# Kernel tuning notes

Hardware: AMD Instinct MI355X
Metric: run time of the kernel (lower is better)

The kernel has to match this reference:

```python
import jax, jax.numpy as jnp
import numpy as np

N = 50000      # nodes
E = 800000     # edges (avg degree 16)
B = 8          # graphs in batch
H = 128        # hidden (message_passer out_channels)
FF = 64        # fourier_feat_dim -> fourier features have dim 2*FF
REPEATS = 4    # repeats_training
OUT = 4        # output_dim
IN_X = 5
IN_MASK = 3

def _fourier(x, M):
    # https://arxiv.org/pdf/2106.02795.pdf : [cos(xM), sin(xM)] / sqrt(2F)
    p = x @ M
    return jnp.concatenate([jnp.cos(p), jnp.sin(p)], axis=-1) / jnp.sqrt(2.0 * M.shape[1])

def _seg_mean(v, idx, n):
    s = jax.ops.segment_sum(v, idx, num_segments=n)
    c = jax.ops.segment_sum(jnp.ones((v.shape[0],), v.dtype), idx, num_segments=n)
    return s / jnp.maximum(c, 1.0)[:, None]

def setup_inputs() -> dict:
    key = jax.random.key(0)
    ks = jax.random.split(key, 16)
    x = jax.random.normal(ks[0], (N, IN_X), jnp.float32)
    x_mask = jax.random.bernoulli(ks[1], 0.1, (N, IN_MASK)).astype(jnp.float32)
    edge_index = jax.random.randint(ks[2], (2, E), 0, N)
    edge_attr = jax.random.normal(ks[3], (E, 3), jnp.float32)
    pos = jax.random.uniform(ks[4], (N, 2), jnp.float32)
    batch = jnp.sort(jax.random.randint(ks[5], (N,), 0, B))
    sampling_points = jax.random.uniform(ks[6], (2,), jnp.float32)
    fourier_mat = jax.random.normal(ks[7], (2, FF), jnp.float32)  # learnable, init N(0,1)
    W_enc = jax.random.normal(ks[8], (IN_X + IN_MASK, H), jnp.float32) * 0.1
    b_enc = jnp.zeros((H,), jnp.float32)
    W_msg = jax.random.normal(ks[9], (2 * H + 3, H), jnp.float32) * 0.05
    b_msg = jnp.zeros((H,), jnp.float32)
    W_upd = jax.random.normal(ks[10], (4 * H, H), jnp.float32) * 0.05
    b_upd = jnp.zeros((H,), jnp.float32)
    W_dec = jax.random.normal(ks[11], (H, OUT), jnp.float32) * 0.1
    b_dec = jnp.zeros((OUT,), jnp.float32)
    return dict(x=x, x_mask=x_mask, edge_index=edge_index, edge_attr=edge_attr,
                pos=pos, batch=batch, sampling_points=sampling_points,
                fourier_mat=fourier_mat, W_enc=W_enc, b_enc=b_enc,
                W_msg=W_msg, b_msg=b_msg, W_upd=W_upd, b_upd=b_upd,
                W_dec=W_dec, b_dec=b_dec)

def reference(x, x_mask, edge_index, edge_attr, pos, batch, sampling_points,
              fourier_mat, W_enc, b_enc, W_msg, b_msg, W_upd, b_upd, W_dec, b_dec):
    bc = x_mask[:, -1]                                   # 0/1 BC flag
    x_full = jnp.concatenate([x, x_mask], axis=1)        # x = concat([x, x_mask])
    keys_ff = _fourier(pos, fourier_mat)                 # input fourier features [N, 2F]
    h = jax.nn.relu(x_full @ W_enc + b_enc)              # encoder -> [N, H]

    # x_BC: scatter-mean over BC nodes per graph (computed once)
    bc_sum = jax.ops.segment_sum(h * bc[:, None], batch, num_segments=B)
    bc_cnt = jax.ops.segment_sum(bc, batch, num_segments=B)
    x_BC = bc_sum / jnp.maximum(bc_cnt, 1.0)[:, None]    # [B, H]

    x_graph = _seg_mean(h, batch, B)                     # global_mean_pool [B, H]
    src, dst = edge_index[0], edge_index[1]
    deg = jnp.maximum(jax.ops.segment_sum(jnp.ones((E,), h.dtype), dst, num_segments=N), 1.0)

    for _ in range(REPEATS):  # repeated message passing
        m = jax.nn.relu(jnp.concatenate([h[src], h[dst], edge_attr], axis=1) @ W_msg + b_msg)
        agg = jax.ops.segment_sum(m, dst, num_segments=N) / deg[:, None]  # scatter-mean
        upd_in = jnp.concatenate([h, agg, x_graph[batch], x_BC[batch]], axis=1)
        h = h + jax.nn.relu(upd_in @ W_upd + b_upd)
        x_graph = _seg_mean(h, batch, B)                 # re-pool each repeat

    decoded = h @ W_dec + b_dec                          # [N, OUT]

    # kernelized fourier-feature interpolation at the sampling point
    q = _fourier(sampling_points, fourier_mat)           # [2F]
    nq = q / jnp.linalg.norm(q)
    nk = keys_ff / jnp.linalg.norm(keys_ff, axis=1, keepdims=True)
    vals_sum = h.sum(axis=0)                             # [H]
    kwv = nk.T @ h                                       # [2F, H]
    ks_sum = nk.sum(axis=0)                              # [2F]
    enc = (vals_sum + nq @ kwv) / (N + nq @ ks_sum)      # [H]
    U_sampled = enc @ W_dec + b_dec                      # [OUT]
    # pack (U_sampled, decoded) into one array: row 0 = sampled point, rows 1: = nodes
    return jnp.concatenate([U_sampled[None, :], decoded], axis=0)
```

## Files before the change

kernel.cpp:

```cpp
#include <hip/hip_runtime.h>
#include <math.h>

#define Nn 50000
#define Ee 800000
#define Bb 8
#define ROUNDS 4
#define KWVB 512
#define SCB 196
#define AP 40
#define HP 132
#define KS 40
#define HTT 136
#define NBK 196
#define P1B 391
#define CHUNK 2047

typedef __attribute__((ext_vector_type(8))) short bf16x8;
typedef __attribute__((ext_vector_type(4))) float f32x4;

__device__ inline short f2bf(float f) {
  union { float f; unsigned u; } v; v.f = f;
  unsigned r = v.u + 0x7fff + ((v.u >> 16) & 1);
  return (short)(r >> 16);
}
__device__ inline float bf2f(short s) {
  union { float f; unsigned u; } v; v.u = ((unsigned)(unsigned short)s) << 16;
  return v.f;
}

__global__ __launch_bounds__(256) void encode_seg(
    const float* __restrict__ x, const float* __restrict__ xm,
    const int* __restrict__ batch, const float* __restrict__ W,
    const float* __restrict__ b, float* __restrict__ h,
    float* __restrict__ gsum, float* __restrict__ gcnt,
    float* __restrict__ bcsum, float* __restrict__ bccnt) {
  __shared__ float xs5[128 * 5];
  __shared__ float xm3[128 * 3];
  __shared__ float ls[Bb * 128];
  __shared__ float lb[Bb * 128];
  __shared__ float lc[Bb], lbc[Bb];
  const int t = threadIdx.x;
  const int nBase = blockIdx.x * 128;
  const int j = t & 127, half = t >> 7;
  const int base5 = nBase * 5, base3 = nBase * 3;
  for (int q = t; q < 640; q += 256) xs5[q] = (base5 + q < Nn * 5) ? x[base5 + q] : 0.f;
  for (int q = t; q < 384; q += 256) xm3[q] = (base3 + q < Nn * 3) ? xm[base3 + q] : 0.f;
  for (int q = t; q < Bb * 128; q += 256) { ls[q] = 0.f; lb[q] = 0.f; }
  if (t < Bb) { lc[t] = 0.f; lbc[t] = 0.f; }
  float Wcol[8];
#pragma unroll
  for (int k = 0; k < 8; k++) Wcol[k] = W[k * 128 + j];
  const float bj = b[j];
  __syncthreads();
  int curb = -1;
  float runh = 0.f, runb = 0.f, runc = 0.f, runbc = 0.f;
  for (int kk = 0; kk < 64; kk++) {
    int i = nBase + kk * 2 + half;
    if (i >= Nn) break;
    int li = i - nBase;
    float acc = bj;
#pragma unroll
    for (int k = 0; k < 5; k++) acc = fmaf(xs5[li * 5 + k], Wcol[k], acc);
#pragma unroll
    for (int k = 0; k < 3; k++) acc = fmaf(xm3[li * 3 + k], Wcol[5 + k], acc);
    float v = fmaxf(acc, 0.f);
    h[(size_t)i * 128 + j] = v;
    float bc = xm3[li * 3 + 2];
    int g = batch[i];
    if (g != curb) {
      if (curb >= 0) {
        atomicAdd(&ls[curb * 128 + j], runh);
        atomicAdd(&lb[curb * 128 + j], runb);
        if (j == 0) { atomicAdd(&lc[curb], runc); atomicAdd(&lbc[curb], runbc); }
      }
      curb = g; runh = runb = runc = runbc = 0.f;
    }
    runh += v; runb += v * bc;
    if (j == 0) { runc += 1.f; runbc += bc; }
  }
  if (curb >= 0) {
    atomicAdd(&ls[curb * 128 + j], runh);
    atomicAdd(&lb[curb * 128 + j], runb);
    if (j == 0) { atomicAdd(&lc[curb], runc); atomicAdd(&lbc[curb], runbc); }
  }
  __syncthreads();
  for (int q = t; q < Bb * 128; q += 256) {
    float a = ls[q], c = lb[q];
    if (a != 0.f) atomicAdd(&gsum[q], a);
    if (c != 0.f) atomicAdd(&bcsum[q], c);
  }
  if (t < Bb) { atomicAdd(&gcnt[t], lc[t]); atomicAdd(&bccnt[t], lbc[t]); }
}

__global__ __launch_bounds__(256) void bkt_cnt(
    const int* __restrict__ ei, int* __restrict__ bktcnt,
    const float* __restrict__ Wm, const float* __restrict__ Wu,
    short* __restrict__ Wmt_h, short* __restrict__ Wmt_l,
    short* __restrict__ Wut_h, short* __restrict__ Wut_l) {
  __shared__ int hist[NBK];
  int t = threadIdx.x;
  int idx = blockIdx.x * 256 + t;
  if (idx < 32768) {
    int k = idx & 127, n = (idx >> 7) & 127, y = idx >> 14;
    float w = Wm[(size_t)(y * 128 + k) * 128 + n];
    short hi = f2bf(w);
    Wmt_h[idx] = hi;
    Wmt_l[idx] = f2bf(w - bf2f(hi));
  } else if (idx < 65536) {
    int j = idx - 32768;
    int k = j & 255, n = j >> 8;
    float w = Wu[(size_t)k * 128 + n];
    short hi = f2bf(w);
    Wut_h[j] = hi;
    Wut_l[j] = f2bf(w - bf2f(hi));
  }
  for (int q = t; q < NBK; q += 256) hist[q] = 0;
  __syncthreads();
  int base = blockIdx.x * CHUNK;
  int end = base + CHUNK < Ee ? base + CHUNK : Ee;
  for (int e = base + t; e < end; e += 256) atomicAdd(&hist[ei[Ee + e] >> 8], 1);
  __syncthreads();
  for (int q = t; q < NBK; q += 256)
    if (hist[q]) atomicAdd(&bktcnt[q], hist[q]);
}
__global__ __launch_bounds__(256) void bkt_scan(const int* __restrict__ bktcnt,
                                                int* __restrict__ bktbase,
                                                int* __restrict__ bktcur) {
  __shared__ int s[256];
  int t = threadIdx.x;
  int v = (t < NBK) ? bktcnt[t] : 0;
  s[t] = v;
  __syncthreads();
  for (int off = 1; off < 256; off <<= 1) {
    int x = (t >= off) ? s[t - off] : 0;
    __syncthreads();
    s[t] += x;
    __syncthreads();
  }
  int ex = s[t] - v;
  if (t < NBK) { bktbase[t] = ex; bktcur[t] = ex; }
  if (t == NBK - 1) bktbase[NBK] = ex + v;
}
__global__ __launch_bounds__(256) void bkt_part(
    const int* __restrict__ ei, const float* __restrict__ ea,
    int* __restrict__ bktcur, int2* __restrict__ recA,
    unsigned char* __restrict__ dlo) {
  __shared__ int hist[NBK], lbase[NBK], lcur[NBK];
  int t = threadIdx.x;
  for (int q = t; q < NBK; q += 256) hist[q] = 0;
  __syncthreads();
  int base = blockIdx.x * CHUNK;
  int end = base + CHUNK < Ee ? base + CHUNK : Ee;
  for (int e = base + t; e < end; e += 256) atomicAdd(&hist[ei[Ee + e] >> 8], 1);
  __syncthreads();
  for (int q = t; q < NBK; q += 256) {
    int c = hist[q];
    lbase[q] = c ? atomicAdd(&bktcur[q], c) : 0;
    lcur[q] = 0;
  }
  __syncthreads();
  for (int e = base + t; e < end; e += 256) {
    int d = ei[Ee + e];
    int bk = d >> 8;
    int p = lbase[bk] + atomicAdd(&lcur[bk], 1);
    unsigned r0 = (unsigned)ei[e] |
                  ((unsigned)(unsigned short)f2bf(ea[3 * (size_t)e + 0]) << 16);
    unsigned r1 = (unsigned)(unsigned short)f2bf(ea[3 * (size_t)e + 1]) |
                  ((unsigned)(unsigned short)f2bf(ea[3 * (size_t)e + 2]) << 16);
    recA[p] = make_int2((int)r0, (int)r1);
    dlo[p] = (unsigned char)(d & 255);
  }
}
__global__ __launch_bounds__(256) void dst_cnt_bsum(
    const int* __restrict__ bktbase, const unsigned char* __restrict__ dlo,
    int* __restrict__ cnt, int* __restrict__ bsum) {
  __shared__ int hh[256];
  __shared__ int wsum[4];
  int t = threadIdx.x;
  hh[t] = 0;
  __syncthreads();
  int b = blockIdx.x;
  int lo = bktbase[b], hi = bktbase[b + 1];
  for (int i = lo + t; i < hi; i += 256) atomicAdd(&hh[dlo[i]], 1);
  __syncthreads();
  int d = b * 256 + t;
  int v = hh[t];
  if (d < Nn) cnt[d] = v;
#pragma unroll
  for (int off = 32; off > 0; off >>= 1) v += __shfl_down(v, off);
  if ((t & 63) == 0) wsum[t >> 6] = v;
  __syncthreads();
  if (t == 0) bsum[b] = wsum[0] + wsum[1] + wsum[2] + wsum[3];
}
__global__ __launch_bounds__(256) void scan_top_kernel(const int* __restrict__ bsum,
                                                       int* __restrict__ boff) {
  __shared__ int s[256];
  int t = threadIdx.x;
  int v = (t < SCB) ? bsum[t] : 0;
  s[t] = v;
  __syncthreads();
  for (int off = 1; off < 256; off <<= 1) {
    int x = (t >= off) ? s[t - off] : 0;
    __syncthreads();
    s[t] += x;
    __syncthreads();
  }
  boff[t] = s[t] - v;
}
__global__ __launch_bounds__(256) void apply_fin(
    const int* __restrict__ cnt, const int* __restrict__ boff,
    const int* __restrict__ bktbase, const int2* __restrict__ recA,
    const unsigned char* __restrict__ dlo,
    int* __restrict__ rowptr, float* __restrict__ invdeg,
    int2* __restrict__ rec) {
  __shared__ int s[256];
  __shared__ int cur[256];
  int t = threadIdx.x, b = blockIdx.x;
  int i = b * 256 + t;
  int v = (i < Nn) ? cnt[i] : 0;
  s[t] = v;
  __syncthreads();
  for (int off = 1; off < 256; off <<= 1) {
    int x = (t >= off) ? s[t - off] : 0;
    __syncthreads();
    s[t] += x;
    __syncthreads();
  }
  int ex = boff[b] + s[t] - v;
  if (i < Nn) {
    rowptr[i] = ex;
    invdeg[i] = 1.0f / fmaxf((float)v, 1.0f);
    if (i == Nn - 1) rowptr[Nn] = ex + v;
  }
  cur[t] = ex;
  __syncthreads();
  int lo = bktbase[b], hi = bktbase[b + 1];
  for (int ii = lo + t; ii < hi; ii += 256) {
    int dl = dlo[ii];
    int p = atomicAdd(&cur[dl], 1);
    rec[p] = recA[ii];
  }
}

__global__ __launch_bounds__(256) void proj_mfma(
    const float* __restrict__ h, const short* __restrict__ Wth,
    unsigned char* __restrict__ hs8, unsigned short* __restrict__ hdbf,
    const float* __restrict__ bcsum, const float* __restrict__ bccnt,
    const float* __restrict__ bu, const float* __restrict__ Wu,
    float* __restrict__ gbst, const float* __restrict__ gsum_in,
    const float* __restrict__ gcnt, float* __restrict__ gb_out) {
  __shared__ short Ah_s[64 * AP];
  __shared__ short Bh_s[256 * AP];
  const int t = threadIdx.x;
  const int nBase = blockIdx.x * 64;
  const int wave = t >> 6, lane = t & 63;
  const int ml = lane & 15, quad = lane >> 4;
  const int ko = quad * 8;

  if (blockIdx.x < Bb) {
    float* xgs = (float*)Bh_s;
    const int g = blockIdx.x;
    if (t < 128) xgs[t] = bcsum[g * 128 + t] / fmaxf(bccnt[g], 1.f);
    __syncthreads();
    if (t < 128) {
      float a = bu[t];
#pragma unroll 4
      for (int k = 0; k < 128; k++) a = fmaf(xgs[k], Wu[(size_t)(384 + k) * 128 + t], a);
      gbst[g * 128 + t] = a;
    }
    __syncthreads();
    if (t < 128) xgs[t] = gsum_in[g * 128 + t] / fmaxf(gcnt[g], 1.f);
    __syncthreads();
    if (t < 128) {
      float a = gbst[g * 128 + t];
#pragma unroll 4
      for (int k = 0; k < 128; k++) a = fmaf(xgs[k], Wu[(size_t)(256 + k) * 128 + t], a);
      gb_out[g * 128 + t] = a;
    }
  }

  f32x4 acc[4][4];
#pragma unroll
  for (int yn = 0; yn < 4; yn++)
#pragma unroll
    for (int mt = 0; mt < 4; mt++)
#pragma unroll
      for (int q = 0; q < 4; q++) acc[yn][mt][q] = 0.f;

  const int arow = t >> 2;
  const int kq = (t & 3) * 8;
  const int nd0 = nBase + arow;
  const int nn = nd0 < Nn ? nd0 : Nn - 1;

  for (int c = 0; c < 4; c++) {
    const int k0 = c * 32;
    const float* p = &h[(size_t)nn * 128 + k0 + kq];
    float4 u0 = *(const float4*)(p + 0);
    float4 u1 = *(const float4*)(p + 4);
    const bf16x8 w0 = *(const bf16x8*)&Wth[(size_t)t * 128 + k0];
    const bf16x8 w1 = *(const bf16x8*)&Wth[(size_t)t * 128 + k0 + 8];
    const bf16x8 w2 = *(const bf16x8*)&Wth[(size_t)t * 128 + k0 + 16];
    const bf16x8 w3 = *(const bf16x8*)&Wth[(size_t)t * 128 + k0 + 24];
    float xs[8] = {u0.x, u0.y, u0.z, u0.w, u1.x, u1.y, u1.z, u1.w};
    bf16x8 vh0;
#pragma unroll
    for (int j = 0; j < 8; j++) vh0[j] = f2bf(xs[j]);
    __syncthreads();
    *(bf16x8*)&Ah_s[arow * AP + kq] = vh0;
    *(bf16x8*)&Bh_s[t * AP + 0] = w0;
    *(bf16x8*)&Bh_s[t * AP + 8] = w1;
    *(bf16x8*)&Bh_s[t * AP + 16] = w2;
    *(bf16x8*)&Bh_s[t * AP + 24] = w3;
    __syncthreads();
#pragma unroll
    for (int mt = 0; mt < 4; mt++) {
      const int ar = (mt * 16 + ml) * AP + ko;
      bf16x8 ah = *(const bf16x8*)&Ah_s[ar];
#pragma unroll
      for (int y = 0; y < 2; y++) {
#pragma unroll
        for (int nt = 0; nt < 2; nt++) {
          const int br = (y * 128 + wave * 32 + nt * 16 + ml) * AP + ko;
          bf16x8 bh = *(const bf16x8*)&Bh_s[br];
          acc[y * 2 + nt][mt] = __builtin_amdgcn_mfma_f32_16x16x32_bf16(ah, bh, acc[y * 2 + nt][mt], 0, 0, 0);
        }
      }
    }
  }
#pragma unroll
  for (int nt = 0; nt < 2; nt++) {
    const int ch = wave * 32 + nt * 16 + ml;
#pragma unroll
    for (int mt = 0; mt < 4; mt++) {
#pragma unroll
      for (int q = 0; q < 4; q++) {
        int nd = nBase + mt * 16 + quad * 4 + q;
        if (nd < Nn) {
          int pk = __builtin_amdgcn_cvt_pk_fp8_f32(acc[nt][mt][q], acc[nt][mt][q], 0, false);
          hs8[(size_t)nd * 128 + ch] = (unsigned char)(pk & 0xff);
          hdbf[(size_t)nd * 128 + ch] = (unsigned short)f2bf(acc[2 + nt][mt][q]);
        }
      }
    }
  }
}

__global__ __launch_bounds__(256) void agg_kernel(
    const unsigned char* __restrict__ hs8, const unsigned short* __restrict__ hdbf,
    unsigned short* __restrict__ aggbf, const int2* __restrict__ rec,
    const int* __restrict__ rowptr, const float* __restrict__ invdeg,
    const float* __restrict__ Wm, const float* __restrict__ bm,
    const float* __restrict__ Wu, const float* __restrict__ gbst,
    const float* __restrict__ gsum_in, const float* __restrict__ gcnt,
    float* __restrict__ gb_out, int dogb) {
  __shared__ float xgs[128];
  int t = threadIdx.x;
  if (dogb && blockIdx.x < Bb) {
    const int g = blockIdx.x;
    if (t < 128) xgs[t] = gsum_in[g * 128 + t] / fmaxf(gcnt[g], 1.f);
    __syncthreads();
    if (t < 128) {
      float a = gbst[g * 128 + t];
#pragma unroll 4
      for (int k = 0; k < 128; k++) a = fmaf(xgs[k], Wu[(size_t)(256 + k) * 128 + t], a);
      gb_out[g * 128 + t] = a;
    }
  }
  int hw = t >> 5, lane = t & 31;
  int v = blockIdx.x * 8 + hw;
  if (v >= Nn) return;
  int c0 = lane * 4;
  const float4 We0 = *(const float4*)&Wm[(size_t)256 * 128 + c0];
  const float4 We1 = *(const float4*)&Wm[(size_t)257 * 128 + c0];
  const float4 We2 = *(const float4*)&Wm[(size_t)258 * 128 + c0];
  const float4 b4  = *(const float4*)&bm[c0];
  const ushort4 hd4 = *(const ushort4*)&hdbf[(size_t)v * 128 + c0];
// ... 33 lines not shown
  }
  if (e < r1) {
    int2 q0 = rec[e];
    int s0 = q0.x & 0xffff;
    unsigned hr0 = *(const unsigned*)&hs8[(size_t)s0 * 128 + c0];
    float e00 = bf2f((short)(q0.x >> 16));
    float e01 = bf2f((short)(q0.y & 0xffff));
    float e02 = bf2f((short)(q0.y >> 16));
    float h0x = __builtin_amdgcn_cvt_f32_fp8(hr0, 0);
    float h0y = __builtin_amdgcn_cvt_f32_fp8(hr0, 1);
    float h0z = __builtin_amdgcn_cvt_f32_fp8(hr0, 2);
    float h0w = __builtin_amdgcn_cvt_f32_fp8(hr0, 3);
    ax += fmaxf(fmaf(e00, We0.x, fmaf(e01, We1.x, fmaf(e02, We2.x, h0x + bx))), 0.f);
    ay += fmaxf(fmaf(e00, We0.y, fmaf(e01, We1.y, fmaf(e02, We2.y, h0y + by))), 0.f);
    az += fmaxf(fmaf(e00, We0.z, fmaf(e01, We1.z, fmaf(e02, We2.z, h0z + bz))), 0.f);
    aw += fmaxf(fmaf(e00, We0.w, fmaf(e01, We1.w, fmaf(e02, We2.w, h0w + bw))), 0.f);
  }
  const float idg = invdeg[v];
  ushort4 o;
  o.x = (unsigned short)f2bf((ax + ax2) * idg);
  o.y = (unsigned short)f2bf((ay + ay2) * idg);
  o.z = (unsigned short)f2bf((az + az2) * idg);
  o.w = (unsigned short)f2bf((aw + aw2) * idg);
  *(ushort4*)&aggbf[(size_t)v * 128 + c0] = o;
}

__global__ __launch_bounds__(256) void updg_proj(
    float* __restrict__ h, const unsigned short* __restrict__ aggbf,
    const int* __restrict__ batch,
    const short* __restrict__ Wth, const short* __restrict__ Wtl,
    const float* __restrict__ gb, float* __restrict__ gsum_out,
    const short* __restrict__ Wmth, unsigned char* __restrict__ hs8,
    unsigned short* __restrict__ hdbf, int doproj) {
  __shared__ short ms[15360];
  __shared__ float gbs[Bb * 128];
  __shared__ float ls[Bb * 128];
  short* Ah_s = ms;
  short* Al_s = ms + 64 * AP;
  short* Bh_s = ms + 2 * 64 * AP;
  short* Bl_s = ms + 2 * 64 * AP + 128 * AP;
  short* hnT  = ms;

  const int t = threadIdx.x;
  const int nBase = blockIdx.x * 64;
  *(float4*)&gbs[t * 4] = *(const float4*)&gb[t * 4];
#pragma unroll
  for (int q = 0; q < 4; q++) ls[t + q * 256] = 0.f;

  const int wave = t >> 6, lane = t & 63;
  const int ml = lane & 15, quad = lane >> 4;
  const int ko = quad * 8;

  f32x4 acc[2][4];
#pragma unroll
  for (int nt = 0; nt < 2; nt++)
#pragma unroll
    for (int mt = 0; mt < 4; mt++)
#pragma unroll
      for (int q = 0; q < 4; q++) acc[nt][mt][q] = 0.f;

  const int arow = t >> 2;
  const int kq = (t & 3) * 8;
  const int brow = t >> 1;
  const int kc = (t & 1) * 16;
  const int nd0 = nBase + arow;
  const int nn = nd0 < Nn ? nd0 : Nn - 1;

  for (int c = 0; c < 8; c++) {
    const int k0 = c * 32;
    bf16x8 vh0, vl0;
    if (c < 4) {
      const float* p = &h[(size_t)nn * 128 + k0 + kq];
      float4 u0 = *(const float4*)(p + 0);
      float4 u1 = *(const float4*)(p + 4);
      float xs[8] = {u0.x, u0.y, u0.z, u0.w, u1.x, u1.y, u1.z, u1.w};
#pragma unroll
      for (int j = 0; j < 8; j++) {
        short hi = f2bf(xs[j]);
        vh0[j] = hi; vl0[j] = f2bf(xs[j] - bf2f(hi));
      }
    } else {
      vh0 = *(const bf16x8*)&aggbf[(size_t)nn * 128 + (c - 4) * 32 + kq];
    }
    const bf16x8 gb0 = *(const bf16x8*)&Wth[(size_t)brow * 256 + k0 + kc];
    const bf16x8 gb1 = *(const bf16x8*)&Wth[(size_t)brow * 256 + k0 + kc + 8];
    const bf16x8 gl0 = *(const bf16x8*)&Wtl[(size_t)brow * 256 + k0 + kc];
    const bf16x8 gl1 = *(const bf16x8*)&Wtl[(size_t)brow * 256 + k0 + kc + 8];
    __syncthreads();
    *(bf16x8*)&Ah_s[arow * AP + kq] = vh0;
    if (c < 4) *(bf16x8*)&Al_s[arow * AP + kq] = vl0;
    *(bf16x8*)&Bh_s[brow * AP + kc] = gb0;
    *(bf16x8*)&Bh_s[brow * AP + kc + 8] = gb1;
    *(bf16x8*)&Bl_s[brow * AP + kc] = gl0;
    *(bf16x8*)&Bl_s[brow * AP + kc + 8] = gl1;
    __syncthreads();
    if (c < 4) {
#pragma unroll
      for (int mt = 0; mt < 4; mt++) {
        const int ar = (mt * 16 + ml) * AP + ko;
        bf16x8 ah = *(const bf16x8*)&Ah_s[ar];
        bf16x8 al = *(const bf16x8*)&Al_s[ar];
#pragma unroll
        for (int nt = 0; nt < 2; nt++) {
          const int br = (wave * 32 + nt * 16 + ml) * AP + ko;
          bf16x8 bh = *(const bf16x8*)&Bh_s[br];
          bf16x8 bl = *(const bf16x8*)&Bl_s[br];
          acc[nt][mt] = __builtin_amdgcn_mfma_f32_16x16x32_bf16(ah, bh, acc[nt][mt], 0, 0, 0);
          acc[nt][mt] = __builtin_amdgcn_mfma_f32_16x16x32_bf16(ah, bl, acc[nt][mt], 0, 0, 0);
          acc[nt][mt] = __builtin_amdgcn_mfma_f32_16x16x32_bf16(al, bh, acc[nt][mt], 0, 0, 0);
        }
      }
    } else {
#pragma unroll
      for (int mt = 0; mt < 4; mt++) {
        const int ar = (mt * 16 + ml) * AP + ko;
        bf16x8 ah = *(const bf16x8*)&Ah_s[ar];
#pragma unroll
        for (int nt = 0; nt < 2; nt++) {
          const int br = (wave * 32 + nt * 16 + ml) * AP + ko;
          bf16x8 bh = *(const bf16x8*)&Bh_s[br];
          bf16x8 bl = *(const bf16x8*)&Bl_s[br];
          acc[nt][mt] = __builtin_amdgcn_mfma_f32_16x16x32_bf16(ah, bh, acc[nt][mt], 0, 0, 0);
          acc[nt][mt] = __builtin_amdgcn_mfma_f32_16x16x32_bf16(ah, bl, acc[nt][mt], 0, 0, 0);
        }
      }
    }
  }
  __syncthreads();

#pragma unroll
  for (int nt = 0; nt < 2; nt++) {
    const int ch = wave * 32 + nt * 16 + ml;
#pragma unroll
    for (int mt = 0; mt < 4; mt++) {
      int lrb = mt * 16 + quad * 4;
      int rbase = nBase + lrb;
      float runv = 0.f;
      int curb = -1;
#pragma unroll
      for (int q = 0; q < 4; q++) {
        int nd = rbase + q;
        short hv = 0;
        if (nd < Nn) {
          int bi = batch[nd];
          float u = fmaxf(acc[nt][mt][q] + gbs[bi * 128 + ch], 0.f);
          float hn = h[(size_t)nd * 128 + ch] + u;
          h[(size_t)nd * 128 + ch] = hn;
          hv = f2bf(hn);
          if (bi != curb) {
            if (curb >= 0) atomicAdd(&ls[curb * 128 + ch], runv);
            curb = bi;
            runv = 0.f;
          }
          runv += hn;
        }
        hnT[(lrb + q) * HTT + ch] = hv;
      }
      if (curb >= 0) atomicAdd(&ls[curb * 128 + ch], runv);
// ... 238 lines not shown
                              void* d_out, int out_size, void* d_ws, size_t ws_size,
                              hipStream_t stream) {
  const float* x    = (const float*)d_in[0];
  const float* xm   = (const float*)d_in[1];
  const int*   ei   = (const int*)d_in[2];
  const float* ea   = (const float*)d_in[3];
  const float* pos  = (const float*)d_in[4];
  const int*   batch= (const int*)d_in[5];
  const float* sp   = (const float*)d_in[6];
  const float* Fm   = (const float*)d_in[7];
  const float* Wenc = (const float*)d_in[8];
  const float* benc = (const float*)d_in[9];
  const float* Wmsg = (const float*)d_in[10];
  const float* bmsg = (const float*)d_in[11];
  const float* Wupd = (const float*)d_in[12];
  const float* bupd = (const float*)d_in[13];
  const float* Wdec = (const float*)d_in[14];
  const float* bdec = (const float*)d_in[15];
  float* out = (float*)d_out;

  float* ws     = (float*)d_ws;
  float* h      = ws;
  float* agg    = h + (size_t)Nn * 128;
  float* aux    = agg + (size_t)Nn * 128;
  float* invdeg = aux + (size_t)Nn * 128;
  float* gsum   = invdeg + Nn;
  float* gcnt   = gsum + 1024;
  float* bcsum  = gcnt + 8;
  float* bccnt  = bcsum + 1024;
  float* gsumR  = bccnt + 8;
  float* vsum   = gsumR + 4096;
  float* ksum   = vsum + 128;
  int*   bktcnt = (int*)(ksum + 128);
  float* gbst   = (float*)(bktcnt + 196);
  float* gbuf   = gbst + 1024;
  float* kwv    = gbuf + 4096;
  int2*  rec    = (int2*)(kwv + 16384);
  int*   cnt    = (int*)(rec + Ee);
  int*   rowptr = cnt + Nn;
  int*   bsum   = rowptr + Nn + 1;
  int*   boff   = bsum + 256;
  int*   bktbase= boff + 256;
  int*   bktcur = bktbase + 197;
  short* wmt_h  = (short*)(bktcur + 196);
  short* wmt_l  = wmt_h + 32768;
  short* wut_h  = wmt_l + 32768;
  short* wut_l  = wut_h + 32768;
  int2*  recA   = (int2*)(wut_l + 32768);
  unsigned char* dlo = (unsigned char*)(recA + Ee);

  unsigned short* aggbf = (unsigned short*)agg;
  unsigned char*  hs8   = (unsigned char*)aux;
  unsigned short* hdbf  = (unsigned short*)(hs8 + (size_t)Nn * 128);

  hipMemsetAsync(gsum, 0, 6612 * 4, stream);

  bkt_cnt<<<P1B, 256, 0, stream>>>(ei, bktcnt, Wmsg, Wupd,
                                   wmt_h, wmt_l, wut_h, wut_l);
  bkt_scan<<<1, 256, 0, stream>>>(bktcnt, bktbase, bktcur);
  bkt_part<<<P1B, 256, 0, stream>>>(ei, ea, bktcur, recA, dlo);
  dst_cnt_bsum<<<NBK, 256, 0, stream>>>(bktbase, dlo, cnt, bsum);
  scan_top_kernel<<<1, 256, 0, stream>>>(bsum, boff);
  apply_fin<<<NBK, 256, 0, stream>>>(cnt, boff, bktbase, recA, dlo,
                                     rowptr, invdeg, rec);

  const int nb128 = (Nn + 127) / 128;
  const int nb64  = (Nn + 63) / 64;
  encode_seg<<<nb128, 256, 0, stream>>>(x, xm, batch, Wenc, benc, h,
                                        gsum, gcnt, bcsum, bccnt);

  proj_mfma<<<nb64, 256, 0, stream>>>(h, wmt_h, hs8, hdbf,
                                      bcsum, bccnt, bupd, Wupd, gbst,
                                      gsum, gcnt, gbuf);

  for (int r = 0; r < ROUNDS; r++) {
    agg_kernel<<<(Nn + 7) / 8, 256, 0, stream>>>(
        hs8, hdbf, aggbf, rec, rowptr, invdeg, Wmsg, bmsg,
        Wupd, gbst,
        (r == 0) ? gsum : (gsumR + (size_t)(r - 1) * 1024), gcnt,
        gbuf + (size_t)r * 1024, (r >= 1) ? 1 : 0);
    updg_proj<<<nb64, 256, 0, stream>>>(
        h, aggbf, batch, wut_h, wut_l,
        gbuf + (size_t)r * 1024, gsumR + (size_t)r * 1024,
        wmt_h, hs8, hdbf, (r < ROUNDS - 1) ? 1 : 0);
  }

  kwv_kernel<<<KWVB, 256, 0, stream>>>(h, pos, Fm, Wdec, bdec, agg, ksum, out);
  kwv_reduce<<<64, 256, 0, stream>>>(agg, kwv);
  final_kernel<<<1, 128, 0, stream>>>(sp, Fm, kwv, gsumR + 3 * 1024, ksum,
                                      Wdec, bdec, out);
}
```

Measured before the change: 617.8 us.

## Stage full A tile in LDS once and load weight fragments directly from global

In proj_mfma and updg_proj, the per-32-k-chunk loop that staged both the activation and weight tiles into LDS with two barriers per chunk is replaced. The whole 64x128 activation tile (hi/lo bf16 split) is now written to padded LDS once, and the MFMA B fragments are read straight from global (L2-cached) weights. proj_mfma also splits its two 128-wide outputs into a sequential loop to cut accumulator registers. This removes most __syncthreads and LDS weight traffic, in exchange for uncoalesced per-lane global weight loads and more LDS per block.

Result: no change. 626.4 us (+1.4%).

```diff
diff --git a/kernel.cpp b/kernel.cpp
--- a/kernel.cpp
+++ b/kernel.cpp
@@ -7,7 +7,6 @@
 #define ROUNDS 4
 #define KWVB 512
 #define SCB 196
-#define AP 40
 #define HP 132
 #define KS 40
 #define HTT 136
@@ -249,8 +248,7 @@
     const float* __restrict__ bu, const float* __restrict__ Wu,
     float* __restrict__ gbst, const float* __restrict__ gsum_in,
     const float* __restrict__ gcnt, float* __restrict__ gb_out) {
-  __shared__ short Ah_s[64 * AP];
-  __shared__ short Bh_s[256 * AP];
+  __shared__ short Ah[64 * HTT];
   const int t = threadIdx.x;
   const int nBase = blockIdx.x * 64;
   const int wave = t >> 6, lane = t & 63;
@@ -258,7 +256,7 @@
   const int ko = quad * 8;
 
   if (blockIdx.x < Bb) {
-    float* xgs = (float*)Bh_s;
+    float* xgs = (float*)Ah;
     const int g = blockIdx.x;
     if (t < 128) xgs[t] = bcsum[g * 128 + t] / fmaxf(bccnt[g], 1.f);
     __syncthreads();
@@ -277,68 +275,76 @@
       for (int k = 0; k < 128; k++) a = fmaf(xgs[k], Wu[(size_t)(256 + k) * 128 + t], a);
       gb_out[g * 128 + t] = a;
     }
-  }
-
-  f32x4 acc[4][4];
-#pragma unroll
-  for (int yn = 0; yn < 4; yn++)
-#pragma unroll
-    for (int mt = 0; mt < 4; mt++)
-#pragma unroll
-      for (int q = 0; q < 4; q++) acc[yn][mt][q] = 0.f;
-
-  const int arow = t >> 2;
-  const int kq = (t & 3) * 8;
-  const int nd0 = nBase + arow;
+    __syncthreads();
+  }
+
+  const int ar = t >> 2;
+  const int cb = (t & 3) * 32;
+  const int nd0 = nBase + ar;
   const int nn = nd0 < Nn ? nd0 : Nn - 1;
 
-  for (int c = 0; c < 4; c++) {
-    const int k0 = c * 32;
-    const float* p = &h[(size_t)nn * 128 + k0 + kq];
-    float4 u0 = *(const float4*)(p + 0);
-    float4 u1 = *(const float4*)(p + 4);
-    const bf16x8 w0 = *(const bf16x8*)&Wth[(size_t)t * 128 + k0];
-    const bf16x8 w1 = *(const bf16x8*)&Wth[(size_t)t * 128 + k0 + 8];
-    const bf16x8 w2 = *(const bf16x8*)&Wth[(size_t)t * 128 + k0 + 16];
-    const bf16x8 w3 = *(const bf16x8*)&Wth[(size_t)t * 128 + k0 + 24];
-    float xs[8] = {u0.x, u0.y, u0.z, u0.w, u1.x, u1.y, u1.z, u1.w};
-    bf16x8 vh0;
-#pragma unroll
-    for (int j = 0; j < 8; j++) vh0[j] = f2bf(xs[j]);
-    __syncthreads();
-    *(bf16x8*)&Ah_s[arow * AP + kq] = vh0;
-    *(bf16x8*)&Bh_s[t * AP + 0] = w0;
-    *(bf16x8*)&Bh_s[t * AP + 8] = w1;
-    *(bf16x8*)&Bh_s[t * AP + 16] = w2;
-    *(bf16x8*)&Bh_s[t * AP + 24] = w3;
-    __syncthreads();
-#pragma unroll
-    for (int mt = 0; mt < 4; mt++) {
-      const int ar = (mt * 16 + ml) * AP + ko;
-      bf16x8 ah = *(const bf16x8*)&Ah_s[ar];
-#pragma unroll
-      for (int y = 0; y < 2; y++) {
-#pragma unroll
-        for (int nt = 0; nt < 2; nt++) {
-          const int br = (y * 128 + wave * 32 + nt * 16 + ml) * AP + ko;
-          bf16x8 bh = *(const bf16x8*)&Bh_s[br];
-          acc[y * 2 + nt][mt] = __builtin_amdgcn_mfma_f32_16x16x32_bf16(ah, bh, acc[y * 2 + nt][mt], 0, 0, 0);
+  {
+    const float* p = &h[(size_t)nn * 128 + cb];
+#pragma unroll
+    for (int jj = 0; jj < 4; jj++) {
+      float4 u0 = *(const float4*)(p + jj * 8);
+      float4 u1 = *(const float4*)(p + jj * 8 + 4);
+      float xs[8] = {u0.x, u0.y, u0.z, u0.w, u1.x, u1.y, u1.z, u1.w};
+      bf16x8 vh;
+#pragma unroll
+      for (int j = 0; j < 8; j++) vh[j] = f2bf(xs[j]);
+      *(bf16x8*)&Ah[ar * HTT + cb + jj * 8] = vh;
+    }
+  }
+  __syncthreads();
+
+#pragma unroll 1
+  for (int y = 0; y < 2; y++) {
+    f32x4 pacc[2][4];
+#pragma unroll
+    for (int nt = 0; nt < 2; nt++)
+#pragma unroll
+      for (int mt = 0; mt < 4; mt++)
+#pragma unroll
+        for (int q = 0; q < 4; q++) pacc[nt][mt][q] = 0.f;
+#pragma unroll
+    for (int c = 0; c < 4; c++) {
+      const bf16x8 b0 = *(const bf16x8*)&Wth[(size_t)(y * 128 + wave * 32 + ml) * 128 + c * 32 + ko];
+      const bf16x8 b1 = *(const bf16x8*)&Wth[(size_t)(y * 128 + wave * 32 + 16 + ml) * 128 + c * 32 + ko];
+#pragma unroll
+      for (int mt = 0; mt < 4; mt++) {
+        bf16x8 ah = *(const bf16x8*)&Ah[(mt * 16 + ml) * HTT + c * 32 + ko];
+        pacc[0][mt] = __builtin_amdgcn_mfma_f32_16x16x32_bf16(ah, b0, pacc[0][mt], 0, 0, 0);
+        pacc[1][mt] = __builtin_amdgcn_mfma_f32_16x16x32_bf16(ah, b1, pacc[1][mt], 0, 0, 0);
+      }
+    }
+    if (y == 0) {
+#pragma unroll
+      for (int nt = 0; nt < 2; nt++) {
+        const int ch = wave * 32 + nt * 16 + ml;
+#pragma unroll
+        for (int mt = 0; mt < 4; mt++) {
+#pragma unroll
+          for (int q = 0; q < 4; q++) {
+            int nd = nBase + mt * 16 + quad * 4 + q;
+            if (nd < Nn) {
+              int pk = __builtin_amdgcn_cvt_pk_fp8_f32(pacc[nt][mt][q], pacc[nt][mt][q], 0, false);
+              hs8[(size_t)nd * 128 + ch] = (unsigned char)(pk & 0xff);
+            }
+          }
         }
       }
-    }
-  }
-#pragma unroll
-  for (int nt = 0; nt < 2; nt++) {
-    const int ch = wave * 32 + nt * 16 + ml;
-#pragma unroll
-    for (int mt = 0; mt < 4; mt++) {
-#pragma unroll
-      for (int q = 0; q < 4; q++) {
-        int nd = nBase + mt * 16 + quad * 4 + q;
-        if (nd < Nn) {
-          int pk = __builtin_amdgcn_cvt_pk_fp8_f32(acc[nt][mt][q], acc[nt][mt][q], 0, false);
-          hs8[(size_t)nd * 128 + ch] = (unsigned char)(pk & 0xff);
-          hdbf[(size_t)nd * 128 + ch] = (unsigned short)f2bf(acc[2 + nt][mt][q]);
+    } else {
+#pragma unroll
+      for (int nt = 0; nt < 2; nt++) {
+        const int ch = wave * 32 + nt * 16 + ml;
+#pragma unroll
+        for (int mt = 0; mt < 4; mt++) {
+#pragma unroll
+          for (int q = 0; q < 4; q++) {
+            int nd = nBase + mt * 16 + quad * 4 + q;
+            if (nd < Nn) hdbf[(size_t)nd * 128 + ch] = (unsigned short)f2bf(pacc[nt][mt][q]);
+          }
         }
       }
     }
@@ -441,14 +447,12 @@
     const float* __restrict__ gb, float* __restrict__ gsum_out,
     const short* __restrict__ Wmth, unsigned char* __restrict__ hs8,
     unsigned short* __restrict__ hdbf, int doproj) {
-  __shared__ short ms[15360];
+  __shared__ short ms[2 * 64 * HTT];
   __shared__ float gbs[Bb * 128];
   __shared__ float ls[Bb * 128];
-  short* Ah_s = ms;
-  short* Al_s = ms + 64 * AP;
-  short* Bh_s = ms + 2 * 64 * AP;
-  short* Bl_s = ms + 2 * 64 * AP + 128 * AP;
-  short* hnT  = ms;
+  short* Ah = ms;
+  short* Al = ms + 64 * HTT;
+  short* hnT = ms;
 
   const int t = threadIdx.x;
   const int nBase = blockIdx.x * 64;
@@ -468,71 +472,73 @@
 #pragma unroll
       for (int q = 0; q < 4; q++) acc[nt][mt][q] = 0.f;
 
-  const int arow = t >> 2;
-  const int kq = (t & 3) * 8;
-  const int brow = t >> 1;
-  const int kc = (t & 1) * 16;
-  const int nd0 = nBase + arow;
+  const int ar = t >> 2;
+  const int cb = (t & 3) * 32;
+  const int nd0 = nBase + ar;
   const int nn = nd0 < Nn ? nd0 : Nn - 1;
 
-  for (int c = 0; c < 8; c++) {
-    const int k0 = c * 32;
-    bf16x8 vh0, vl0;
-    if (c < 4) {
-      const float* p = &h[(size_t)nn * 128 + k0 + kq];
-      float4 u0 = *(const float4*)(p + 0);
-      float4 u1 = *(const float4*)(p + 4);
+  {
+    const float* p = &h[(size_t)nn * 128 + cb];
+#pragma unroll
+    for (int jj = 0; jj < 4; jj++) {
+      float4 u0 = *(const float4*)(p + jj * 8);
+      float4 u1 = *(const float4*)(p + jj * 8 + 4);
       float xs[8] = {u0.x, u0.y, u0.z, u0.w, u1.x, u1.y, u1.z, u1.w};
+      bf16x8 vh, vl;
 #pragma unroll
       for (int j = 0; j < 8; j++) {
         short hi = f2bf(xs[j]);
-        vh0[j] = hi; vl0[j] = f2bf(xs[j] - bf2f(hi));
-      }
-    } else {
-      vh0 = *(const bf16x8*)&aggbf[(size_t)nn * 128 + (c - 4) * 32 + kq];
-    }
-    const bf16x8 gb0 = *(const bf16x8*)&Wth[(size_t)brow * 256 + k0 + kc];
-    const bf16x8 gb1 = *(const bf16x8*)&Wth[(size_t)brow * 256 + k0 + kc + 8];
-    const bf16x8 gl0 = *(const bf16x8*)&Wtl[(size_t)brow * 256 + k0 + kc];
-    const bf16x8 gl1 = *(const bf16x8*)&Wtl[(size_t)brow * 256 + k0 + kc + 8];
-    __syncthreads();
-    *(bf16x8*)&Ah_s[arow * AP + kq] = vh0;
-    if (c < 4) *(bf16x8*)&Al_s[arow * AP + kq] = vl0;
-    *(bf16x8*)&Bh_s[brow * AP + kc] = gb0;
-    *(bf16x8*)&Bh_s[brow * AP + kc + 8] = gb1;
-    *(bf16x8*)&Bl_s[brow * AP + kc] = gl0;
-    *(bf16x8*)&Bl_s[brow * AP + kc + 8] = gl1;
-    __syncthreads();
-    if (c < 4) {
-#pragma unroll
-      for (int mt = 0; mt < 4; mt++) {
-        const int ar = (mt * 16 + ml) * AP + ko;
-        bf16x8 ah = *(const bf16x8*)&Ah_s[ar];
-        bf16x8 al = *(const bf16x8*)&Al_s[ar];
-#pragma unroll
-        for (int nt = 0; nt < 2; nt++) {
-          const int br = (wave * 32 + nt * 16 + ml) * AP + ko;
-          bf16x8 bh = *(const bf16x8*)&Bh_s[br];
-          bf16x8 bl = *(const bf16x8*)&Bl_s[br];
-          acc[nt][mt] = __builtin_amdgcn_mfma_f32_16x16x32_bf16(ah, bh, acc[nt][mt], 0, 0, 0);
-          acc[nt][mt] = __builtin_amdgcn_mfma_f32_16x16x32_bf16(ah, bl, acc[nt][mt], 0, 0, 0);
-          acc[nt][mt] = __builtin_amdgcn_mfma_f32_16x16x32_bf16(al, bh, acc[nt][mt], 0, 0, 0);
-        }
-      }
-    } else {
-#pragma unroll
-      for (int mt = 0; mt < 4; mt++) {
-        const int ar = (mt * 16 + ml) * AP + ko;
-        bf16x8 ah = *(const bf16x8*)&Ah_s[ar];
-#pragma unroll
-        for (int nt = 0; nt < 2; nt++) {
-          const int br = (wave * 32 + nt * 16 + ml) * AP + ko;
-          bf16x8 bh = *(const bf16x8*)&Bh_s[br];
-          bf16x8 bl = *(const bf16x8*)&Bl_s[br];
-          acc[nt][mt] = __builtin_amdgcn_mfma_f32_16x16x32_bf16(ah, bh, acc[nt][mt], 0, 0, 0);
-          acc[nt][mt] = __builtin_amdgcn_mfma_f32_16x16x32_bf16(ah, bl, acc[nt][mt], 0, 0, 0);
-        }
-      }
+        vh[j] = hi; vl[j] = f2bf(xs[j] - bf2f(hi));
+      }
+      *(bf16x8*)&Ah[ar * HTT + cb + jj * 8] = vh;
+      *(bf16x8*)&Al[ar * HTT + cb + jj * 8] = vl;
+    }
+  }
+  __syncthreads();
+
+#pragma unroll
+  for (int c = 0; c < 4; c++) {
+    const int k0 = c * 32;
+    bf16x8 bh0 = *(const bf16x8*)&Wth[(size_t)(wave * 32 + ml) * 256 + k0 + ko];
+    bf16x8 bl0 = *(const bf16x8*)&Wtl[(size_t)(wave * 32 + ml) * 256 + k0 + ko];
+    bf16x8 bh1 = *(const bf16x8*)&Wth[(size_t)(wave * 32 + 16 + ml) * 256 + k0 + ko];
+    bf16x8 bl1 = *(const bf16x8*)&Wtl[(size_t)(wave * 32 + 16 + ml) * 256 + k0 + ko];
+#pragma unroll
+    for (int mt = 0; mt < 4; mt++) {
+      bf16x8 ah = *(const bf16x8*)&Ah[(mt * 16 + ml) * HTT + k0 + ko];
+      bf16x8 al = *(const bf16x8*)&Al[(mt * 16 + ml) * HTT + k0 + ko];
+      acc[0][mt] = __builtin_amdgcn_mfma_f32_16x16x32_bf16(ah, bh0, acc[0][mt], 0, 0, 0);
+      acc[0][mt] = __builtin_amdgcn_mfma_f32_16x16x32_bf16(ah, bl0, acc[0][mt], 0, 0, 0);
+      acc[0][mt] = __builtin_amdgcn_mfma_f32_16x16x32_bf16(al, bh0, acc[0][mt], 0, 0, 0);
+      acc[1][mt] = __builtin_amdgcn_mfma_f32_16x16x32_bf16(ah, bh1, acc[1][mt], 0, 0, 0);
+      acc[1][mt] = __builtin_amdgcn_mfma_f32_16x16x32_bf16(ah, bl1, acc[1][mt], 0, 0, 0);
+      acc[1][mt] = __builtin_amdgcn_mfma_f32_16x16x32_bf16(al, bh1, acc[1][mt], 0, 0, 0);
+    }
+  }
+  __syncthreads();
+
+  {
+    const unsigned short* pa = &aggbf[(size_t)nn * 128 + cb];
+#pragma unroll
+    for (int jj = 0; jj < 4; jj++)
+      *(bf16x8*)&Ah[ar * HTT + cb + jj * 8] = *(const bf16x8*)(pa + jj * 8);
+  }
+  __syncthreads();
+
+#pragma unroll
+  for (int c = 4; c < 8; c++) {
+    const int k0 = c * 32, ka = (c - 4) * 32;
+    bf16x8 bh0 = *(const bf16x8*)&Wth[(size_t)(wave * 32 + ml) * 256 + k0 + ko];
+    bf16x8 bl0 = *(const bf16x8*)&Wtl[(size_t)(wave * 32 + ml) * 256 + k0 + ko];
+    bf16x8 bh1 = *(const bf16x8*)&Wth[(size_t)(wave * 32 + 16 + ml) * 256 + k0 + ko];
+    bf16x8 bl1 = *(const bf16x8*)&Wtl[(size_t)(wave * 32 + 16 + ml) * 256 + k0 + ko];
+#pragma unroll
+    for (int mt = 0; mt < 4; mt++) {
+      bf16x8 ah = *(const bf16x8*)&Ah[(mt * 16 + ml) * HTT + ka + ko];
+      acc[0][mt] = __builtin_amdgcn_mfma_f32_16x16x32_bf16(ah, bh0, acc[0][mt], 0, 0, 0);
+      acc[0][mt] = __builtin_amdgcn_mfma_f32_16x16x32_bf16(ah, bl0, acc[0][mt], 0, 0, 0);
+      acc[1][mt] = __builtin_amdgcn_mfma_f32_16x16x32_bf16(ah, bh1, acc[1][mt], 0, 0, 0);
+      acc[1][mt] = __builtin_amdgcn_mfma_f32_16x16x32_bf16(ah, bl1, acc[1][mt], 0, 0, 0);
     }
   }
   __syncthreads();
```

## Merge CSR build kernels with encoder and projection to cut launches

Applied to the files above, without the earlier changes.

Merges the edge bucket counting into the encoder launch and the bucket partitioning into the projection launch, using disjoint block ranges inside each fused kernel. The single-block scan kernels are removed and their prefix scans are recomputed redundantly in every block of the consuming kernels. bktcur moves into the memset region so it starts at zero. This drops four kernel launches and lets independent CSR work share the GPU with node work, at the cost of repeated small scans and extra shared memory in each fused kernel.

Result: faster. 598.1 us, median of 2 (-3.2%).

```diff
diff --git a/kernel.cpp b/kernel.cpp
--- a/kernel.cpp
+++ b/kernel.cpp
@@ -28,19 +28,50 @@
   return v.f;
 }
 
-__global__ __launch_bounds__(256) void encode_seg(
+__global__ __launch_bounds__(256) void csr_enc(
+    const int* __restrict__ ei, int* __restrict__ bktcnt,
+    const float* __restrict__ Wm, const float* __restrict__ Wu,
+    short* __restrict__ Wmt_h, short* __restrict__ Wmt_l,
+    short* __restrict__ Wut_h, short* __restrict__ Wut_l,
     const float* __restrict__ x, const float* __restrict__ xm,
     const int* __restrict__ batch, const float* __restrict__ W,
     const float* __restrict__ b, float* __restrict__ h,
     float* __restrict__ gsum, float* __restrict__ gcnt,
     float* __restrict__ bcsum, float* __restrict__ bccnt) {
+  __shared__ int hist[NBK];
   __shared__ float xs5[128 * 5];
   __shared__ float xm3[128 * 3];
   __shared__ float ls[Bb * 128];
   __shared__ float lb[Bb * 128];
   __shared__ float lc[Bb], lbc[Bb];
   const int t = threadIdx.x;
-  const int nBase = blockIdx.x * 128;
+  if (blockIdx.x < P1B) {
+    int idx = blockIdx.x * 256 + t;
+    if (idx < 32768) {
+      int k = idx & 127, n = (idx >> 7) & 127, y = idx >> 14;
+      float w = Wm[(size_t)(y * 128 + k) * 128 + n];
+      short hi = f2bf(w);
+      Wmt_h[idx] = hi;
+      Wmt_l[idx] = f2bf(w - bf2f(hi));
+    } else if (idx < 65536) {
+      int j = idx - 32768;
+      int k = j & 255, n = j >> 8;
+      float w = Wu[(size_t)k * 128 + n];
+      short hi = f2bf(w);
+      Wut_h[j] = hi;
+      Wut_l[j] = f2bf(w - bf2f(hi));
+    }
+    for (int q = t; q < NBK; q += 256) hist[q] = 0;
+    __syncthreads();
+    int base = blockIdx.x * CHUNK;
+    int end = base + CHUNK < Ee ? base + CHUNK : Ee;
+    for (int e = base + t; e < end; e += 256) atomicAdd(&hist[ei[Ee + e] >> 8], 1);
+    __syncthreads();
+    for (int q = t; q < NBK; q += 256)
+      if (hist[q]) atomicAdd(&bktcnt[q], hist[q]);
+    return;
+  }
+  const int nBase = (blockIdx.x - P1B) * 128;
   const int j = t & 127, half = t >> 7;
   const int base5 = nBase * 5, base3 = nBase * 3;
   for (int q = t; q < 640; q += 256) xs5[q] = (base5 + q < Nn * 5) ? x[base5 + q] : 0.f;
@@ -92,174 +123,65 @@
   if (t < Bb) { atomicAdd(&gcnt[t], lc[t]); atomicAdd(&bccnt[t], lbc[t]); }
 }
 
-__global__ __launch_bounds__(256) void bkt_cnt(
-    const int* __restrict__ ei, int* __restrict__ bktcnt,
-    const float* __restrict__ Wm, const float* __restrict__ Wu,
-    short* __restrict__ Wmt_h, short* __restrict__ Wmt_l,
-    short* __restrict__ Wut_h, short* __restrict__ Wut_l) {
-  __shared__ int hist[NBK];
-  int t = threadIdx.x;
-  int idx = blockIdx.x * 256 + t;
-  if (idx < 32768) {
-    int k = idx & 127, n = (idx >> 7) & 127, y = idx >> 14;
-    float w = Wm[(size_t)(y * 128 + k) * 128 + n];
-    short hi = f2bf(w);
-    Wmt_h[idx] = hi;
-    Wmt_l[idx] = f2bf(w - bf2f(hi));
-  } else if (idx < 65536) {
-    int j = idx - 32768;
-    int k = j & 255, n = j >> 8;
-    float w = Wu[(size_t)k * 128 + n];
-    short hi = f2bf(w);
-    Wut_h[j] = hi;
-    Wut_l[j] = f2bf(w - bf2f(hi));
-  }
-  for (int q = t; q < NBK; q += 256) hist[q] = 0;
-  __syncthreads();
-  int base = blockIdx.x * CHUNK;
-  int end = base + CHUNK < Ee ? base + CHUNK : Ee;
-  for (int e = base + t; e < end; e += 256) atomicAdd(&hist[ei[Ee + e] >> 8], 1);
-  __syncthreads();
-  for (int q = t; q < NBK; q += 256)
-    if (hist[q]) atomicAdd(&bktcnt[q], hist[q]);
-}
-__global__ __launch_bounds__(256) void bkt_scan(const int* __restrict__ bktcnt,
-                                                int* __restrict__ bktbase,
-                                                int* __restrict__ bktcur) {
-  __shared__ int s[256];
-  int t = threadIdx.x;
-  int v = (t < NBK) ? bktcnt[t] : 0;
-  s[t] = v;
-  __syncthreads();
-  for (int off = 1; off < 256; off <<= 1) {
-    int x = (t >= off) ? s[t - off] : 0;
-    __syncthreads();
-    s[t] += x;
-    __syncthreads();
-  }
-  int ex = s[t] - v;
-  if (t < NBK) { bktbase[t] = ex; bktcur[t] = ex; }
-  if (t == NBK - 1) bktbase[NBK] = ex + v;
-}
-__global__ __launch_bounds__(256) void bkt_part(
+__global__ __launch_bounds__(256) void part_proj(
     const int* __restrict__ ei, const float* __restrict__ ea,
-    int* __restrict__ bktcur, int2* __restrict__ recA,
-    unsigned char* __restrict__ dlo) {
-  __shared__ int hist[NBK], lbase[NBK], lcur[NBK];
-  int t = threadIdx.x;
-  for (int q = t; q < NBK; q += 256) hist[q] = 0;
-  __syncthreads();
-  int base = blockIdx.x * CHUNK;
-  int end = base + CHUNK < Ee ? base + CHUNK : Ee;
-  for (int e = base + t; e < end; e += 256) atomicAdd(&hist[ei[Ee + e] >> 8], 1);
-  __syncthreads();
-  for (int q = t; q < NBK; q += 256) {
-    int c = hist[q];
-    lbase[q] = c ? atomicAdd(&bktcur[q], c) : 0;
-    lcur[q] = 0;
-  }
-  __syncthreads();
-  for (int e = base + t; e < end; e += 256) {
-    int d = ei[Ee + e];
-    int bk = d >> 8;
-    int p = lbase[bk] + atomicAdd(&lcur[bk], 1);
-    unsigned r0 = (unsigned)ei[e] |
-                  ((unsigned)(unsigned short)f2bf(ea[3 * (size_t)e + 0]) << 16);
-    unsigned r1 = (unsigned)(unsigned short)f2bf(ea[3 * (size_t)e + 1]) |
-                  ((unsigned)(unsigned short)f2bf(ea[3 * (size_t)e + 2]) << 16);
-    recA[p] = make_int2((int)r0, (int)r1);
-    dlo[p] = (unsigned char)(d & 255);
-  }
-}
-__global__ __launch_bounds__(256) void dst_cnt_bsum(
-    const int* __restrict__ bktbase, const unsigned char* __restrict__ dlo,
-    int* __restrict__ cnt, int* __restrict__ bsum) {
-  __shared__ int hh[256];
-  __shared__ int wsum[4];
-  int t = threadIdx.x;
-  hh[t] = 0;
-  __syncthreads();
-  int b = blockIdx.x;
-  int lo = bktbase[b], hi = bktbase[b + 1];
-  for (int i = lo + t; i < hi; i += 256) atomicAdd(&hh[dlo[i]], 1);
-  __syncthreads();
-  int d = b * 256 + t;
-  int v = hh[t];
-  if (d < Nn) cnt[d] = v;
-#pragma unroll
-  for (int off = 32; off > 0; off >>= 1) v += __shfl_down(v, off);
-  if ((t & 63) == 0) wsum[t >> 6] = v;
-  __syncthreads();
-  if (t == 0) bsum[b] = wsum[0] + wsum[1] + wsum[2] + wsum[3];
-}
-__global__ __launch_bounds__(256) void scan_top_kernel(const int* __restrict__ bsum,
-                                                       int* __restrict__ boff) {
-  __shared__ int s[256];
-  int t = threadIdx.x;
-  int v = (t < SCB) ? bsum[t] : 0;
-  s[t] = v;
-  __syncthreads();
-  for (int off = 1; off < 256; off <<= 1) {
-    int x = (t >= off) ? s[t - off] : 0;
-    __syncthreads();
-    s[t] += x;
-    __syncthreads();
-  }
-  boff[t] = s[t] - v;
-}
-__global__ __launch_bounds__(256) void apply_fin(
-    const int* __restrict__ cnt, const int* __restrict__ boff,
-    const int* __restrict__ bktbase, const int2* __restrict__ recA,
-    const unsigned char* __restrict__ dlo,
-    int* __restrict__ rowptr, float* __restrict__ invdeg,
-    int2* __restrict__ rec) {
-  __shared__ int s[256];
-  __shared__ int cur[256];
-  int t = threadIdx.x, b = blockIdx.x;
-  int i = b * 256 + t;
-  int v = (i < Nn) ? cnt[i] : 0;
-  s[t] = v;
-  __syncthreads();
-  for (int off = 1; off < 256; off <<= 1) {
-    int x = (t >= off) ? s[t - off] : 0;
-    __syncthreads();
-    s[t] += x;
-    __syncthreads();
-  }
-  int ex = boff[b] + s[t] - v;
-  if (i < Nn) {
-    rowptr[i] = ex;
-    invdeg[i] = 1.0f / fmaxf((float)v, 1.0f);
-    if (i == Nn - 1) rowptr[Nn] = ex + v;
-  }
-  cur[t] = ex;
-  __syncthreads();
-  int lo = bktbase[b], hi = bktbase[b + 1];
-  for (int ii = lo + t; ii < hi; ii += 256) {
-    int dl = dlo[ii];
-    int p = atomicAdd(&cur[dl], 1);
-    rec[p] = recA[ii];
-  }
-}
-
-__global__ __launch_bounds__(256) void proj_mfma(
+    const int* __restrict__ bktcnt, int* __restrict__ bktcur,
+    int2* __restrict__ recA, unsigned char* __restrict__ dlo,
     const float* __restrict__ h, const short* __restrict__ Wth,
     unsigned char* __restrict__ hs8, unsigned short* __restrict__ hdbf,
     const float* __restrict__ bcsum, const float* __restrict__ bccnt,
     const float* __restrict__ bu, const float* __restrict__ Wu,
     float* __restrict__ gbst, const float* __restrict__ gsum_in,
     const float* __restrict__ gcnt, float* __restrict__ gb_out) {
+  __shared__ int hist[NBK], lbase[NBK], lcur[NBK], bb[NBK], sS[256];
   __shared__ short Ah_s[64 * AP];
   __shared__ short Bh_s[256 * AP];
   const int t = threadIdx.x;
-  const int nBase = blockIdx.x * 64;
+  if (blockIdx.x < P1B) {
+    int v = (t < NBK) ? bktcnt[t] : 0;
+    sS[t] = v;
+    __syncthreads();
+    for (int off = 1; off < 256; off <<= 1) {
+      int xo = (t >= off) ? sS[t - off] : 0;
+      __syncthreads();
+      sS[t] += xo;
+      __syncthreads();
+    }
+    if (t < NBK) bb[t] = sS[t] - v;
+    for (int q = t; q < NBK; q += 256) hist[q] = 0;
+    __syncthreads();
+    int base = blockIdx.x * CHUNK;
+    int end = base + CHUNK < Ee ? base + CHUNK : Ee;
+    for (int e = base + t; e < end; e += 256) atomicAdd(&hist[ei[Ee + e] >> 8], 1);
+    __syncthreads();
+    for (int q = t; q < NBK; q += 256) {
+      int c = hist[q];
+      lbase[q] = c ? (bb[q] + atomicAdd(&bktcur[q], c)) : 0;
+      lcur[q] = 0;
+    }
+    __syncthreads();
+    for (int e = base + t; e < end; e += 256) {
+      int d = ei[Ee + e];
+      int bk = d >> 8;
+      int p = lbase[bk] + atomicAdd(&lcur[bk], 1);
+      unsigned r0 = (unsigned)ei[e] |
+                    ((unsigned)(unsigned short)f2bf(ea[3 * (size_t)e + 0]) << 16);
+      unsigned r1 = (unsigned)(unsigned short)f2bf(ea[3 * (size_t)e + 1]) |
+                    ((unsigned)(unsigned short)f2bf(ea[3 * (size_t)e + 2]) << 16);
+      recA[p] = make_int2((int)r0, (int)r1);
+      dlo[p] = (unsigned char)(d & 255);
+    }
+    return;
+  }
+  const int pbid = blockIdx.x - P1B;
+  const int nBase = pbid * 64;
   const int wave = t >> 6, lane = t & 63;
   const int ml = lane & 15, quad = lane >> 4;
   const int ko = quad * 8;
 
-  if (blockIdx.x < Bb) {
+  if (pbid < Bb) {
     float* xgs = (float*)Bh_s;
-    const int g = blockIdx.x;
+    const int g = pbid;
     if (t < 128) xgs[t] = bcsum[g * 128 + t] / fmaxf(bccnt[g], 1.f);
     __syncthreads();
     if (t < 128) {
@@ -342,6 +264,96 @@
         }
       }
     }
+  }
+}
+
+__global__ __launch_bounds__(256) void dst_cnt_bsum(
+    const int* __restrict__ bktcnt, const unsigned char* __restrict__ dlo,
+    int* __restrict__ cnt, int* __restrict__ bsum) {
+  __shared__ int s[256];
+  __shared__ int hh[256];
+  __shared__ int wsum[4];
+  int t = threadIdx.x;
+  int b = blockIdx.x;
+  int vv = (t < NBK) ? bktcnt[t] : 0;
+  s[t] = vv;
+  __syncthreads();
+  for (int off = 1; off < 256; off <<= 1) {
+    int xo = (t >= off) ? s[t - off] : 0;
+    __syncthreads();
+    s[t] += xo;
+    __syncthreads();
+  }
+  int lo = (b == 0) ? 0 : s[b - 1];
+  int hi = s[b];
+  hh[t] = 0;
+  __syncthreads();
+  for (int i = lo + t; i < hi; i += 256) atomicAdd(&hh[dlo[i]], 1);
+  __syncthreads();
+  int d = b * 256 + t;
+  int v = hh[t];
+  if (d < Nn) cnt[d] = v;
+#pragma unroll
+  for (int off = 32; off > 0; off >>= 1) v += __shfl_down(v, off);
+  if ((t & 63) == 0) wsum[t >> 6] = v;
+  __syncthreads();
+  if (t == 0) bsum[b] = wsum[0] + wsum[1] + wsum[2] + wsum[3];
+}
+
+__global__ __launch_bounds__(256) void apply_fin(
+    const int* __restrict__ cnt, const int* __restrict__ bsum,
+    const int* __restrict__ bktcnt, const int2* __restrict__ recA,
+    const unsigned char* __restrict__ dlo,
+    int* __restrict__ rowptr, float* __restrict__ invdeg,
+    int2* __restrict__ rec) {
+  __shared__ int s[256];
+  __shared__ int cur[256];
+  int t = threadIdx.x, b = blockIdx.x;
+  int vb = (t < SCB) ? bsum[t] : 0;
+  s[t] = vb;
+  __syncthreads();
+  for (int off = 1; off < 256; off <<= 1) {
+    int xo = (t >= off) ? s[t - off] : 0;
+    __syncthreads();
+    s[t] += xo;
+    __syncthreads();
+  }
+  int boffb = (b == 0) ? 0 : s[b - 1];
+  __syncthreads();
+  int vk = (t < NBK) ? bktcnt[t] : 0;
+  s[t] = vk;
+  __syncthreads();
+  for (int off = 1; off < 256; off <<= 1) {
+    int xo = (t >= off) ? s[t - off] : 0;
+    __syncthreads();
+    s[t] += xo;
+    __syncthreads();
+  }
+  int lo = (b == 0) ? 0 : s[b - 1];
+  int hi = s[b];
+  __syncthreads();
+  int i = b * 256 + t;
+  int v = (i < Nn) ? cnt[i] : 0;
+  s[t] = v;
+  __syncthreads();
+  for (int off = 1; off < 256; off <<= 1) {
+    int xo = (t >= off) ? s[t - off] : 0;
+    __syncthreads();
+    s[t] += xo;
+    __syncthreads();
+  }
+  int ex = boffb + s[t] - v;
+  if (i < Nn) {
+    rowptr[i] = ex;
+    invdeg[i] = 1.0f / fmaxf((float)v, 1.0f);
+    if (i == Nn - 1) rowptr[Nn] = ex + v;
+  }
+  cur[t] = ex;
+  __syncthreads();
+  for (int ii = lo + t; ii < hi; ii += 256) {
+    int dl = dlo[ii];
+    int p = atomicAdd(&cur[dl], 1);
+    rec[p] = recA[ii];
   }
 }
 
@@ -837,17 +849,15 @@
   float* vsum   = gsumR + 4096;
   float* ksum   = vsum + 128;
   int*   bktcnt = (int*)(ksum + 128);
-  float* gbst   = (float*)(bktcnt + 196);
+  int*   bktcur = bktcnt + 196;
+  float* gbst   = (float*)(bktcur + 196);
   float* gbuf   = gbst + 1024;
   float* kwv    = gbuf + 4096;
   int2*  rec    = (int2*)(kwv + 16384);
   int*   cnt    = (int*)(rec + Ee);
   int*   rowptr = cnt + Nn;
   int*   bsum   = rowptr + Nn + 1;
-  int*   boff   = bsum + 256;
-  int*   bktbase= boff + 256;
-  int*   bktcur = bktbase + 197;
-  short* wmt_h  = (short*)(bktcur + 196);
+  short* wmt_h  = (short*)(bsum + 256);
   short* wmt_l  = wmt_h + 32768;
   short* wut_h  = wmt_l + 32768;
   short* wut_l  = wut_h + 32768;
@@ -858,25 +868,23 @@
   unsigned char*  hs8   = (unsigned char*)aux;
   unsigned short* hdbf  = (unsigned short*)(hs8 + (size_t)Nn * 128);
 
-  hipMemsetAsync(gsum, 0, 6612 * 4, stream);
-
-  bkt_cnt<<<P1B, 256, 0, stream>>>(ei, bktcnt, Wmsg, Wupd,
-                                   wmt_h, wmt_l, wut_h, wut_l);
-  bkt_scan<<<1, 256, 0, stream>>>(bktcnt, bktbase, bktcur);
-  bkt_part<<<P1B, 256, 0, stream>>>(ei, ea, bktcur, recA, dlo);
-  dst_cnt_bsum<<<NBK, 256, 0, stream>>>(bktbase, dlo, cnt, bsum);
-  scan_top_kernel<<<1, 256, 0, stream>>>(bsum, boff);
-  apply_fin<<<NBK, 256, 0, stream>>>(cnt, boff, bktbase, recA, dlo,
-                                     rowptr, invdeg, rec);
+  hipMemsetAsync(gsum, 0, 6808 * 4, stream);
 
   const int nb128 = (Nn + 127) / 128;
   const int nb64  = (Nn + 63) / 64;
-  encode_seg<<<nb128, 256, 0, stream>>>(x, xm, batch, Wenc, benc, h,
-                                        gsum, gcnt, bcsum, bccnt);
-
-  proj_mfma<<<nb64, 256, 0, stream>>>(h, wmt_h, hs8, hdbf,
-                                      bcsum, bccnt, bupd, Wupd, gbst,
-                                      gsum, gcnt, gbuf);
+
+  csr_enc<<<P1B + nb128, 256, 0, stream>>>(
+      ei, bktcnt, Wmsg, Wupd, wmt_h, wmt_l, wut_h, wut_l,
+      x, xm, batch, Wenc, benc, h, gsum, gcnt, bcsum, bccnt);
+
+  part_proj<<<P1B + nb64, 256, 0, stream>>>(
+      ei, ea, bktcnt, bktcur, recA, dlo,
+      h, wmt_h, hs8, hdbf,
+      bcsum, bccnt, bupd, Wupd, gbst, gsum, gcnt, gbuf);
+
+  dst_cnt_bsum<<<NBK, 256, 0, stream>>>(bktcnt, dlo, cnt, bsum);
+  apply_fin<<<NBK, 256, 0, stream>>>(cnt, bsum, bktcnt, recA, dlo,
+                                     rowptr, invdeg, rec);
 
   for (int r = 0; r < ROUNDS; r++) {
     agg_kernel<<<(Nn + 7) / 8, 256, 0, stream>>>(
```
